# Optimization experiments

Measured on AMD Instinct MI355X. Metric: run time of the kernel, lower is better.

## Reference

```python
import jax, jax.numpy as jnp
import numpy as np

NUM_HEADS = 32
NUM_KV_HEADS = 8
HEAD_DIM = 128


def rotate_half(x):
    half = x.shape[-1] // 2
    return jnp.concatenate([-x[..., half:], x[..., :half]], axis=-1)


def setup_inputs() -> dict:
    key = jax.random.key(0)
    ks = jax.random.split(key, 7)
    B, S, H = 2, 2048, 4096
    hidden_states = jax.random.normal(ks[0], (B, S, H), dtype=jnp.float32)
    # rope tables built from real frequencies for realism
    inv_freq = 1.0 / (10000.0 ** (jnp.arange(0, HEAD_DIM, 2, dtype=jnp.float32) / HEAD_DIM))
    pos = jnp.arange(S, dtype=jnp.float32)
    freqs = pos[:, None] * inv_freq[None, :]            # [S, HEAD_DIM//2]
    emb = jnp.concatenate([freqs, freqs], axis=-1)      # [S, HEAD_DIM]
    cos = jnp.broadcast_to(jnp.cos(emb)[None], (B, S, HEAD_DIM)).astype(jnp.float32)
    sin = jnp.broadcast_to(jnp.sin(emb)[None], (B, S, HEAD_DIM)).astype(jnp.float32)
    scale = 0.02
    wq = jax.random.normal(ks[1], (NUM_HEADS * HEAD_DIM, H), dtype=jnp.float32) * scale
    wk = jax.random.normal(ks[2], (NUM_KV_HEADS * HEAD_DIM, H), dtype=jnp.float32) * scale
    wv = jax.random.normal(ks[3], (NUM_KV_HEADS * HEAD_DIM, H), dtype=jnp.float32) * scale
    wo = jax.random.normal(ks[4], (H, NUM_HEADS * HEAD_DIM), dtype=jnp.float32) * scale
    return {"hidden_states": hidden_states, "cos": cos, "sin": sin,
            "wq": wq, "wk": wk, "wv": wv, "wo": wo}


def reference(hidden_states, cos, sin, wq, wk, wv, wo):
    B, S, H = hidden_states.shape
    groups = NUM_HEADS // NUM_KV_HEADS
    scaling = HEAD_DIM ** -0.5

    # QKV projections (nn.Linear, no bias -> x @ W^T)
    q = (hidden_states @ wq.T).reshape(B, S, NUM_HEADS, HEAD_DIM).transpose(0, 2, 1, 3)     # [B,Hq,S,D]
    k = (hidden_states @ wk.T).reshape(B, S, NUM_KV_HEADS, HEAD_DIM).transpose(0, 2, 1, 3)  # [B,Hk,S,D]
    v = (hidden_states @ wv.T).reshape(B, S, NUM_KV_HEADS, HEAD_DIM).transpose(0, 2, 1, 3)  # [B,Hk,S,D]

    # RoPE (HF apply_rotary_pos_emb: cos/sin unsqueezed over head axis)
    c = cos[:, None, :, :]  # [B,1,S,D]
    s = sin[:, None, :, :]
    q = q * c + rotate_half(q) * s
    k = k * c + rotate_half(k) * s

    # GQA: broadcast each KV head to its group of query heads
    k = jnp.repeat(k, groups, axis=1)  # [B,Hq,S,D]
    v = jnp.repeat(v, groups, axis=1)

    # causal SDPA
    scores = jnp.einsum('bhqd,bhkd->bhqk', q, k) * scaling
    causal = jnp.tril(jnp.ones((S, S), dtype=bool))
    neg = jnp.finfo(scores.dtype).min
    scores = jnp.where(causal[None, None], scores, neg)
    probs = jax.nn.softmax(scores, axis=-1)
    attn = jnp.einsum('bhqk,bhkd->bhqd', probs, v)      # [B,Hq,S,D]

    # merge heads + output projection
    attn = attn.transpose(0, 2, 1, 3).reshape(B, S, NUM_HEADS * HEAD_DIM)
    return attn @ wo.T
```

## Files before the change

kernel.cpp:

```cpp
#include <hip/hip_runtime.h>
#include <stdint.h>

typedef __bf16 bf16_t;
typedef __bf16 bf16x8 __attribute__((ext_vector_type(8)));
typedef __bf16 bf16x4 __attribute__((ext_vector_type(4)));
typedef __bf16 bf16x2 __attribute__((ext_vector_type(2)));
typedef float f32x4 __attribute__((ext_vector_type(4)));

#define S_LEN 2048
#define NH 32
#define NKV 8
#define HD 128
#define B_SZ 2
#define HID 4096
#define QKV_N 6144
#define INFF __builtin_inff()
#define QSCALE (0.08838834764831845f * 1.4426950408889634f)

__device__ __forceinline__ void gload_lds16(const void* g, void* l) {
    __builtin_amdgcn_global_load_lds(
        (const __attribute__((address_space(1))) void*)(uintptr_t)g,
        (__attribute__((address_space(3))) void*)(uint32_t)(uintptr_t)l,
        16, 0, 0);
}

__global__ __launch_bounds__(256) void f2b_kernel(const float4* __restrict__ in,
                                                  bf16x4* __restrict__ out, int n4) {
    int i = blockIdx.x * blockDim.x + threadIdx.x;
    if (i >= n4) return;
    float4 v = in[i];
    bf16x4 o = {(bf16_t)v.x, (bf16_t)v.y, (bf16_t)v.z, (bf16_t)v.w};
    out[i] = o;
}

#define SLOT_E 16384

#define GTILE(T, STAGE, VMW) do {                                                         \
    const int _sb = ((T) & 3) * SLOT_E;                                                   \
    bf16x8 af[8], bfr[2];                                                                 \
    _Pragma("unroll") for (int i = 0; i < 8; ++i)                                         \
        af[i] = *(const bf16x8*)&lds[_sb + offA[i]];                                      \
    bfr[0] = *(const bf16x8*)&lds[_sb + 8192 + offB[0]];                                  \
    bfr[1] = *(const bf16x8*)&lds[_sb + 8192 + offB[1]];                                  \
    if (STAGE) {                                                                          \
        const int _ss = (((T) + 3) & 3) * SLOT_E;                                         \
        gload_lds16(sA0, &lds[_ss + ldsO0]); gload_lds16(sA1, &lds[_ss + ldsO1]);         \
        sA0 += 32; sA1 += 32;                                                             \
    }                                                                                     \
    __builtin_amdgcn_s_barrier();                                                         \
    asm volatile("s_waitcnt lgkmcnt(0)" ::: "memory");                                    \
    __builtin_amdgcn_sched_barrier(0);                                                    \
    __builtin_amdgcn_s_setprio(1);                                                        \
    _Pragma("unroll") for (int i = 0; i < 8; ++i) {                                       \
        acc[i][0] = __builtin_amdgcn_mfma_f32_16x16x32_bf16(af[i], bfr[0], acc[i][0], 0, 0, 0); \
        acc[i][1] = __builtin_amdgcn_mfma_f32_16x16x32_bf16(af[i], bfr[1], acc[i][1], 0, 0, 0); \
    }                                                                                     \
    __builtin_amdgcn_s_setprio(0);                                                        \
    __builtin_amdgcn_s_barrier();                                                         \
    bf16x8 bfs[2];                                                                        \
    bfs[0] = *(const bf16x8*)&lds[_sb + 8192 + offB[2]];                                  \
    bfs[1] = *(const bf16x8*)&lds[_sb + 8192 + offB[3]];                                  \
    if (STAGE) {                                                                          \
        const int _ss = (((T) + 3) & 3) * SLOT_E;                                         \
        gload_lds16(sB0, &lds[_ss + 8192 + ldsO0]); gload_lds16(sB1, &lds[_ss + 8192 + ldsO1]); \
        sB0 += 32; sB1 += 32;                                                             \
    }                                                                                     \
    __builtin_amdgcn_s_barrier();                                                         \
    asm volatile("s_waitcnt lgkmcnt(0)" ::: "memory");                                    \
    __builtin_amdgcn_sched_barrier(0);                                                    \
    __builtin_amdgcn_s_setprio(1);                                                        \
    _Pragma("unroll") for (int i = 0; i < 8; ++i) {                                       \
        acc[i][2] = __builtin_amdgcn_mfma_f32_16x16x32_bf16(af[i], bfs[0], acc[i][2], 0, 0, 0); \
        acc[i][3] = __builtin_amdgcn_mfma_f32_16x16x32_bf16(af[i], bfs[1], acc[i][3], 0, 0, 0); \
    }                                                                                     \
    __builtin_amdgcn_s_setprio(0);                                                        \
    if ((VMW) == 8)      asm volatile("s_waitcnt vmcnt(8)" ::: "memory");                 \
    else if ((VMW) == 4) asm volatile("s_waitcnt vmcnt(4)" ::: "memory");                 \
    else if ((VMW) == 0) asm volatile("s_waitcnt vmcnt(0)" ::: "memory");                 \
    __builtin_amdgcn_s_barrier();                                                         \
} while (0)

template<bool F32OUT>
__global__ __launch_bounds__(512, 2) void gemm256(const bf16_t* __restrict__ A,
                                                  const bf16_t* __restrict__ W,
                                                  void* __restrict__ C0,
                                                  void* __restrict__ C1,
                                                  int ld0, int ld1,
                                                  int Nloc, int ldAW, int Kloc) {
    __shared__ __align__(16) bf16_t lds[4 * SLOT_E];
    const int tid = threadIdx.x;
    const int lane = tid & 63;
    const int w = tid >> 6;
    const int wm = w >> 2, wn = w & 3;
    const int l15 = lane & 15, lg = lane >> 4;

    const int z = blockIdx.y;
    void* Cv = z ? C1 : C0;
    const int ldC = z ? ld1 : ld0;
    const int kOff = z * Kloc;

    const int nbx = Nloc >> 8;
    const int cpx = gridDim.x >> 3;
    const int bid = blockIdx.x;
    const int bid2 = (bid & 7) * cpx + (bid >> 3);
    const int m0 = (bid2 / nbx) * 256;
    const int n0 = (bid2 % nbx) * 256;

    const int c0 = tid, c1 = 512 + tid;
    const int rA0 = c0 >> 2, ch0 = (c0 & 3) ^ ((rA0 >> 1) & 3);
    const int rA1 = c1 >> 2, ch1 = (c1 & 3) ^ ((rA1 >> 1) & 3);
    const bf16_t* sA0 = A + (size_t)(m0 + rA0) * ldAW + kOff + ch0 * 8;
    const bf16_t* sA1 = A + (size_t)(m0 + rA1) * ldAW + kOff + ch1 * 8;
    const bf16_t* sB0 = W + (size_t)(n0 + rA0) * ldAW + kOff + ch0 * 8;
    const bf16_t* sB1 = W + (size_t)(n0 + rA1) * ldAW + kOff + ch1 * 8;
    const int ldsO0 = c0 * 8, ldsO1 = c1 * 8;

    int offA[8], offB[4];
    #pragma unroll
    for (int i = 0; i < 8; ++i) {
        int row = wm * 128 + i * 16 + l15;
        offA[i] = row * 32 + ((lg ^ ((row >> 1) & 3)) * 8);
    }
    #pragma unroll
    for (int j = 0; j < 4; ++j) {
        int row = wn * 64 + j * 16 + l15;
        offB[j] = row * 32 + ((lg ^ ((row >> 1) & 3)) * 8);
    }

    #pragma unroll
    for (int tt = 0; tt < 3; ++tt) {
        const int ss = tt * SLOT_E;
        gload_lds16(sA0, &lds[ss + ldsO0]); gload_lds16(sA1, &lds[ss + ldsO1]);
        gload_lds16(sB0, &lds[ss + 8192 + ldsO0]); gload_lds16(sB1, &lds[ss + 8192 + ldsO1]);
        sA0 += 32; sA1 += 32; sB0 += 32; sB1 += 32;
    }
    asm volatile("s_waitcnt vmcnt(8)" ::: "memory");
    __builtin_amdgcn_s_barrier();

    f32x4 acc[8][4] = {};
    const int NT = Kloc >> 5;
    int t = 0;
    for (; t < NT - 3; ++t) GTILE(t, true, 8);
    GTILE(NT - 3, false, 4);
    GTILE(NT - 2, false, 0);
    GTILE(NT - 1, false, -1);

    #pragma unroll
    for (int i = 0; i < 8; ++i)
        #pragma unroll
        for (int jn = 0; jn < 4; ++jn)
            #pragma unroll
            for (int r = 0; r < 4; ++r) {
                int m = m0 + wm * 128 + i * 16 + lg * 4 + r;
                int n = n0 + wn * 64 + jn * 16 + l15;
                float v = acc[i][jn][r];
                if (F32OUT) ((float*)Cv)[(size_t)m * ldC + n] = v;
                else        ((bf16_t*)Cv)[(size_t)m * ldC + n] = (bf16_t)v;
            }
}

__global__ __launch_bounds__(256) void rope_fuse(bf16_t* __restrict__ QKV,
                                                 const bf16_t* __restrict__ P1,
                                                 const float* __restrict__ cosb,
                                                 const float* __restrict__ sinb) {
    int tid = blockIdx.x * blockDim.x + threadIdx.x;
    int d = tid & 63;
    int hg = (tid >> 6) % 48;
    int bs = tid / (64 * 48);
    bf16_t* rowp;
    float x1, x2, posc = 1.f;
    if (hg < 32) {
        rowp = QKV + (size_t)bs * QKV_N + hg * HD;
        x1 = (float)rowp[d];
        x2 = (float)rowp[d + 64];
        posc = QSCALE;
    } else if (hg < 40) {
        int col = HID + (hg - 32) * HD;
        rowp = QKV + (size_t)bs * QKV_N + col;
        const bf16_t* pp = P1 + (size_t)bs * 2048 + (col - HID);
        x1 = (float)rowp[d] + (float)pp[d];
        x2 = (float)rowp[d + 64] + (float)pp[d + 64];
    } else {
        int col = HID + NKV * HD + (hg - 40) * HD;
        rowp = QKV + (size_t)bs * QKV_N + col;
        const bf16_t* pp = P1 + (size_t)bs * 2048 + (col - HID);
        rowp[d]      = (bf16_t)((float)rowp[d]      + (float)pp[d]);
        rowp[d + 64] = (bf16_t)((float)rowp[d + 64] + (float)pp[d + 64]);
        return;
    }
    float c1 = cosb[(size_t)bs * HD + d];
    float s1 = sinb[(size_t)bs * HD + d];
    float c2 = cosb[(size_t)bs * HD + d + 64];
    float s2 = sinb[(size_t)bs * HD + d + 64];
    rowp[d]      = (bf16_t)((x1 * c1 - x2 * s1) * posc);
    rowp[d + 64] = (bf16_t)((x2 * c2 + x1 * s2) * posc);
}

#define PITCH_P 72

__global__ __launch_bounds__(512, 2) void attn_fwd(const bf16_t* __restrict__ QKV,
                                                   bf16_t* __restrict__ O) {
    __shared__ __align__(16) bf16_t Kl[64 * 128];
    __shared__ __align__(16) bf16_t Vt[128 * 64];
    __shared__ __align__(16) bf16_t Pl[8][16 * PITCH_P];
    const int tid = threadIdx.x;
    const int lane = tid & 63;
    const int w = tid >> 6;
    const int l15 = lane & 15, lg = lane >> 4;
    const int pr = blockIdx.x, kvh = blockIdx.y, b = blockIdx.z;
    const int h = kvh * 4 + (w & 3);
    const int rg = w >> 2;

    int krow[2], kch[2];
    #pragma unroll
    for (int jj = 0; jj < 2; ++jj) { int q = jj * 512 + tid; krow[jj] = q >> 4; kch[jj] = q & 15; }
    const int k0v = (tid & 31) * 2;
    const int d0 = (tid >> 5) * 8;
    const int vci = k0v >> 3;
    const int vsub = k0v & 7;

    const bf16_t* Kb0 = QKV + (size_t)(b * S_LEN) * QKV_N + HID + kvh * HD;
    const bf16_t* Vb0 = QKV + (size_t)(b * S_LEN) * QKV_N + HID + NKV * HD + kvh * HD;
    bf16_t* Plw = Pl[w];

    for (int t = 0; t < 2; ++t) {
        const int qt = (t == 0) ? pr : (63 - pr);
        const int q0 = qt * 32;
        const int qrow = q0 + rg * 16 + l15;

        bf16x8 qf[4];
        {
            const bf16_t* qp = QKV + (size_t)(b * S_LEN + qrow) * QKV_N + h * HD;
            #pragma unroll
            for (int c = 0; c < 4; ++c) qf[c] = *(const bf16x8*)&qp[c * 32 + lg * 8];
        }

        f32x4 acc_o[8] = {};
        float mrow = -INFF, lrow = 0.f;
        const int nsteps = qt / 2 + 1;

        bf16x8 kst[2], vst[2];
        #pragma unroll
        for (int jj = 0; jj < 2; ++jj)
            kst[jj] = *(const bf16x8*)&Kb0[(size_t)krow[jj] * QKV_N + kch[jj] * 8];
        vst[0] = *(const bf16x8*)&Vb0[(size_t)(k0v + 0) * QKV_N + d0];
        vst[1] = *(const bf16x8*)&Vb0[(size_t)(k0v + 1) * QKV_N + d0];

        for (int st = 0; st < nsteps; ++st) {
            const int k0 = st * 64;
            __syncthreads();
            #pragma unroll
            for (int jj = 0; jj < 2; ++jj)
                *(bf16x8*)&Kl[krow[jj] * 128 + ((kch[jj] ^ (krow[jj] & 7)) * 8)] = kst[jj];
            #pragma unroll
            for (int j = 0; j < 8; ++j) {
                bf16x2 v2 = { vst[0][j], vst[1][j] };
                *(bf16x2*)&Vt[(d0 + j) * 64 + ((vci ^ j) << 3) + vsub] = v2;
            }
            __syncthreads();
            if (st + 1 < nsteps) {
                const bf16_t* Kb = Kb0 + (size_t)(k0 + 64) * QKV_N;
                const bf16_t* Vb = Vb0 + (size_t)(k0 + 64) * QKV_N;
                #pragma unroll
                for (int jj = 0; jj < 2; ++jj)
                    kst[jj] = *(const bf16x8*)&Kb[(size_t)krow[jj] * QKV_N + kch[jj] * 8];
                vst[0] = *(const bf16x8*)&Vb[(size_t)(k0v + 0) * QKV_N + d0];
                vst[1] = *(const bf16x8*)&Vb[(size_t)(k0v + 1) * QKV_N + d0];
            }
            f32x4 s[4];
            __builtin_amdgcn_s_setprio(1);
            #pragma unroll
            for (int nt = 0; nt < 4; ++nt) {
                s[nt] = (f32x4){0.f, 0.f, 0.f, 0.f};
                const int row = nt * 16 + l15;
                const int rb = row * 128, key = row & 7;
                #pragma unroll
                for (int c = 0; c < 4; ++c) {
                    bf16x8 kf = *(const bf16x8*)&Kl[rb + (((c * 4 + lg) ^ key) * 8)];
                    s[nt] = __builtin_amdgcn_mfma_f32_16x16x32_bf16(kf, qf[c], s[nt], 0, 0, 0);
                }
            }
            __builtin_amdgcn_s_setprio(0);
            if (k0 + 63 > q0 + rg * 16) {
                #pragma unroll
                for (int nt = 0; nt < 4; ++nt)
                    #pragma unroll
                    for (int r = 0; r < 4; ++r) {
                        int k = k0 + nt * 16 + lg * 4 + r;
                        if (k > qrow) s[nt][r] = -INFF;
                    }
            }
            float m0a = fmaxf(fmaxf(s[0][0], s[0][1]), fmaxf(s[0][2], s[0][3]));
            float m1a = fmaxf(fmaxf(s[1][0], s[1][1]), fmaxf(s[1][2], s[1][3]));
            float m2a = fmaxf(fmaxf(s[2][0], s[2][1]), fmaxf(s[2][2], s[2][3]));
            float m3a = fmaxf(fmaxf(s[3][0], s[3][1]), fmaxf(s[3][2], s[3][3]));
            float mx = fmaxf(fmaxf(m0a, m1a), fmaxf(m2a, m3a));
            mx = fmaxf(mx, __shfl_xor(mx, 16));
            mx = fmaxf(mx, __shfl_xor(mx, 32));
            const bool nodefer = !__all(mx <= mrow + 11.5f);
            const float mn = nodefer ? fmaxf(mrow, mx) : mrow;
            float sc = 1.f;
            if (nodefer) sc = exp2f(mrow - mn);
            float rs0 = 0.f, rs1 = 0.f, rs2 = 0.f, rs3 = 0.f;
            #pragma unroll
            for (int nt = 0; nt < 4; ++nt) {
                float e0 = exp2f(s[nt][0] - mn), e1 = exp2f(s[nt][1] - mn);
                float e2 = exp2f(s[nt][2] - mn), e3 = exp2f(s[nt][3] - mn);
                s[nt][0] = e0; s[nt][1] = e1; s[nt][2] = e2; s[nt][3] = e3;
                rs0 += e0; rs1 += e1; rs2 += e2; rs3 += e3;
            }
            float rs = (rs0 + rs1) + (rs2 + rs3);
            rs += __shfl_xor(rs, 16);
            rs += __shfl_xor(rs, 32);
            if (nodefer) { lrow = lrow * sc + rs; mrow = mn; }
            else         { lrow += rs; }
            #pragma unroll
            for (int nt = 0; nt < 4; ++nt) {
                bf16x4 pk = {(bf16_t)s[nt][0], (bf16_t)s[nt][1], (bf16_t)s[nt][2], (bf16_t)s[nt][3]};
                *(bf16x4*)&Plw[l15 * PITCH_P + nt * 16 + lg * 4] = pk;
            }
            if (nodefer) {
                float scb[4];
                #pragma unroll
                for (int r = 0; r < 4; ++r) scb[r] = __shfl(sc, lg * 4 + r);
                #pragma unroll
                for (int nt2 = 0; nt2 < 8; ++nt2)
                    #pragma unroll
                    for (int r = 0; r < 4; ++r) acc_o[nt2][r] *= scb[r];
            }
            __builtin_amdgcn_s_setprio(1);
            #pragma unroll
            for (int kc = 0; kc < 2; ++kc) {
                bf16x8 pf = *(const bf16x8*)&Plw[l15 * PITCH_P + kc * 32 + lg * 8];
                #pragma unroll
                for (int nt2 = 0; nt2 < 8; ++nt2) {
                    const int drow = nt2 * 16 + l15;
                    bf16x8 vf = *(const bf16x8*)&Vt[drow * 64 + (((kc * 4 + lg) ^ (drow & 7)) << 3)];
                    acc_o[nt2] = __builtin_amdgcn_mfma_f32_16x16x32_bf16(pf, vf, acc_o[nt2], 0, 0, 0);
                }
            }
            __builtin_amdgcn_s_setprio(0);
        }
        float lb[4];
        #pragma unroll
        for (int r = 0; r < 4; ++r) lb[r] = __builtin_amdgcn_rcpf(__shfl(lrow, lg * 4 + r));
        #pragma unroll
        for (int nt2 = 0; nt2 < 8; ++nt2)
            #pragma unroll
            for (int r = 0; r < 4; ++r) {
                int q = q0 + rg * 16 + lg * 4 + r;
                int d = nt2 * 16 + l15;
                O[((size_t)(b * S_LEN + q)) * (NH * HD) + h * HD + d] = (bf16_t)(acc_o[nt2][r] * lb[r]);
            }
        __syncthreads();
    }
}

extern "C" void kernel_launch(void* const* d_in, const int* in_sizes, int n_in,
                              void* d_out, int out_size, void* d_ws, size_t ws_size,
                              hipStream_t stream) {
    const float* hs   = (const float*)d_in[0];
    const float* cosb = (const float*)d_in[1];
    const float* sinb = (const float*)d_in[2];
    const float* wq   = (const float*)d_in[3];
    const float* wk   = (const float*)d_in[4];
    const float* wv   = (const float*)d_in[5];
    const float* wo   = (const float*)d_in[6];
    float* out = (float*)d_out;

    const size_t NHS = (size_t)B_SZ * S_LEN * HID;
    const size_t NQKVW = (size_t)QKV_N * HID;
    size_t need = (NHS * 3 + NQKVW * 2) * sizeof(bf16_t);
    if (ws_size < need) return;

    bf16_t* p = (bf16_t*)d_ws;
    bf16_t* hsb  = p; p += NHS;
    bf16_t* wqkv = p; p += NQKVW;
    bf16_t* wob  = p; p += NHS;
    bf16_t* QKVb = p; p += NQKVW;
    bf16_t* Ab   = p; p += NHS;
    bf16_t* P1   = Ab;

    auto cvt = [&](const float* src, bf16_t* dst, size_t n) {
        int n4 = (int)(n / 4);
        f2b_kernel<<<(n4 + 255) / 256, 256, 0, stream>>>((const float4*)src, (bf16x4*)dst, n4);
    };
    cvt(hs, hsb, NHS);
    cvt(wq, wqkv, NHS);
    cvt(wk, wqkv + (size_t)HID * HID, (size_t)NKV * HD * HID);
    cvt(wv, wqkv + (size_t)(HID + NKV * HD) * HID, (size_t)NKV * HD * HID);
    cvt(wo, wob, NHS);

    gemm256<false><<<dim3(256, 1), 512, 0, stream>>>(hsb, wqkv, QKVb, QKVb,
                                                     QKV_N, QKV_N, 4096, HID, HID);
    gemm256<false><<<dim3(128, 2), 512, 0, stream>>>(hsb, wqkv + (size_t)HID * HID,
                                                     QKVb + HID, P1,
                                                     QKV_N, 2048, 2048, HID, 2048);

    int rf_threads = B_SZ * S_LEN * 48 * 64;
    rope_fuse<<<rf_threads / 256, 256, 0, stream>>>(QKVb, P1, cosb, sinb);

    attn_fwd<<<dim3(32, NKV, B_SZ), 512, 0, stream>>>(QKVb, Ab);

    gemm256<true><<<dim3(256, 1), 512, 0, stream>>>(Ab, wob, out, out,
                                                    HID, HID, HID, HID, HID);
}
```

Before: 549.9 us.

## Process two query row-blocks per wave in attention with double-buffered K/V LDS

Each wave now handles 32 query rows (two 16-row MFMA tiles) against the same K/V tile, doubling the query tile per block to 64 and halving the grid. K/V shared-memory tiles are double-buffered, so one of the two barriers per step is removed. This reuses each K/V LDS load across twice as many MFMAs to cut LDS traffic and sync overhead. In exchange it raises register pressure (dropped min-blocks launch bound), grows LDS use, and leaves fewer blocks (256) to fill the GPU.

```diff
diff --git a/kernel.cpp b/kernel.cpp
--- a/kernel.cpp
+++ b/kernel.cpp
@@ -198,11 +198,11 @@
 
 #define PITCH_P 72
 
-__global__ __launch_bounds__(512, 2) void attn_fwd(const bf16_t* __restrict__ QKV,
-                                                   bf16_t* __restrict__ O) {
-    __shared__ __align__(16) bf16_t Kl[64 * 128];
-    __shared__ __align__(16) bf16_t Vt[128 * 64];
-    __shared__ __align__(16) bf16_t Pl[8][16 * PITCH_P];
+__global__ __launch_bounds__(512) void attn_fwd(const bf16_t* __restrict__ QKV,
+                                                bf16_t* __restrict__ O) {
+    __shared__ __align__(16) bf16_t Kl[2][64 * 128];
+    __shared__ __align__(16) bf16_t Vt[2][128 * 64];
+    __shared__ __align__(16) bf16_t Pl[8][2][16 * PITCH_P];
     const int tid = threadIdx.x;
     const int lane = tid & 63;
     const int w = tid >> 6;
@@ -221,23 +221,30 @@
 
     const bf16_t* Kb0 = QKV + (size_t)(b * S_LEN) * QKV_N + HID + kvh * HD;
     const bf16_t* Vb0 = QKV + (size_t)(b * S_LEN) * QKV_N + HID + NKV * HD + kvh * HD;
-    bf16_t* Plw = Pl[w];
+    bf16_t* Pl0 = Pl[w][0];
+    bf16_t* Pl1 = Pl[w][1];
 
     for (int t = 0; t < 2; ++t) {
-        const int qt = (t == 0) ? pr : (63 - pr);
-        const int q0 = qt * 32;
-        const int qrow = q0 + rg * 16 + l15;
-
-        bf16x8 qf[4];
+        const int qt = (t == 0) ? pr : (31 - pr);
+        const int q0 = qt * 64;
+        const int qb0 = q0 + rg * 32;
+        const int qb1 = qb0 + 16;
+        const int qrow0 = qb0 + l15, qrow1 = qb1 + l15;
+
+        bf16x8 qf0[4], qf1[4];
         {
-            const bf16_t* qp = QKV + (size_t)(b * S_LEN + qrow) * QKV_N + h * HD;
-            #pragma unroll
-            for (int c = 0; c < 4; ++c) qf[c] = *(const bf16x8*)&qp[c * 32 + lg * 8];
+            const bf16_t* qp0 = QKV + (size_t)(b * S_LEN + qrow0) * QKV_N + h * HD;
+            const bf16_t* qp1 = QKV + (size_t)(b * S_LEN + qrow1) * QKV_N + h * HD;
+            #pragma unroll
+            for (int c = 0; c < 4; ++c) {
+                qf0[c] = *(const bf16x8*)&qp0[c * 32 + lg * 8];
+                qf1[c] = *(const bf16x8*)&qp1[c * 32 + lg * 8];
+            }
         }
 
-        f32x4 acc_o[8] = {};
-        float mrow = -INFF, lrow = 0.f;
-        const int nsteps = qt / 2 + 1;
+        f32x4 acc0[8] = {}, acc1[8] = {};
+        float mr0 = -INFF, lr0 = 0.f, mr1 = -INFF, lr1 = 0.f;
+        const int nsteps = qt + 1;
 
         bf16x8 kst[2], vst[2];
         #pragma unroll
@@ -248,14 +255,14 @@
 
         for (int st = 0; st < nsteps; ++st) {
             const int k0 = st * 64;
-            __syncthreads();
+            const int p = st & 1;
             #pragma unroll
             for (int jj = 0; jj < 2; ++jj)
-                *(bf16x8*)&Kl[krow[jj] * 128 + ((kch[jj] ^ (krow[jj] & 7)) * 8)] = kst[jj];
+                *(bf16x8*)&Kl[p][krow[jj] * 128 + ((kch[jj] ^ (krow[jj] & 7)) * 8)] = kst[jj];
             #pragma unroll
             for (int j = 0; j < 8; ++j) {
                 bf16x2 v2 = { vst[0][j], vst[1][j] };
-                *(bf16x2*)&Vt[(d0 + j) * 64 + ((vci ^ j) << 3) + vsub] = v2;
+                *(bf16x2*)&Vt[p][(d0 + j) * 64 + ((vci ^ j) << 3) + vsub] = v2;
             }
             __syncthreads();
             if (st + 1 < nsteps) {
@@ -267,90 +274,148 @@
                 vst[0] = *(const bf16x8*)&Vb[(size_t)(k0v + 0) * QKV_N + d0];
                 vst[1] = *(const bf16x8*)&Vb[(size_t)(k0v + 1) * QKV_N + d0];
             }
-            f32x4 s[4];
+            f32x4 s0[4], s1[4];
             __builtin_amdgcn_s_setprio(1);
             #pragma unroll
             for (int nt = 0; nt < 4; ++nt) {
-                s[nt] = (f32x4){0.f, 0.f, 0.f, 0.f};
+                s0[nt] = (f32x4){0.f, 0.f, 0.f, 0.f};
+                s1[nt] = (f32x4){0.f, 0.f, 0.f, 0.f};
                 const int row = nt * 16 + l15;
                 const int rb = row * 128, key = row & 7;
                 #pragma unroll
                 for (int c = 0; c < 4; ++c) {
-                    bf16x8 kf = *(const bf16x8*)&Kl[rb + (((c * 4 + lg) ^ key) * 8)];
-                    s[nt] = __builtin_amdgcn_mfma_f32_16x16x32_bf16(kf, qf[c], s[nt], 0, 0, 0);
+                    bf16x8 kf = *(const bf16x8*)&Kl[p][rb + (((c * 4 + lg) ^ key) * 8)];
+                    s0[nt] = __builtin_amdgcn_mfma_f32_16x16x32_bf16(kf, qf0[c], s0[nt], 0, 0, 0);
+                    s1[nt] = __builtin_amdgcn_mfma_f32_16x16x32_bf16(kf, qf1[c], s1[nt], 0, 0, 0);
                 }
             }
             __builtin_amdgcn_s_setprio(0);
-            if (k0 + 63 > q0 + rg * 16) {
+            if (k0 + 63 > qb0) {
                 #pragma unroll
                 for (int nt = 0; nt < 4; ++nt)
                     #pragma unroll
                     for (int r = 0; r < 4; ++r) {
                         int k = k0 + nt * 16 + lg * 4 + r;
-                        if (k > qrow) s[nt][r] = -INFF;
+                        if (k > qrow0) s0[nt][r] = -INFF;
                     }
             }
-            float m0a = fmaxf(fmaxf(s[0][0], s[0][1]), fmaxf(s[0][2], s[0][3]));
-            float m1a = fmaxf(fmaxf(s[1][0], s[1][1]), fmaxf(s[1][2], s[1][3]));
-            float m2a = fmaxf(fmaxf(s[2][0], s[2][1]), fmaxf(s[2][2], s[2][3]));
-            float m3a = fmaxf(fmaxf(s[3][0], s[3][1]), fmaxf(s[3][2], s[3][3]));
-            float mx = fmaxf(fmaxf(m0a, m1a), fmaxf(m2a, m3a));
-            mx = fmaxf(mx, __shfl_xor(mx, 16));
-            mx = fmaxf(mx, __shfl_xor(mx, 32));
-            const bool nodefer = !__all(mx <= mrow + 11.5f);
-            const float mn = nodefer ? fmaxf(mrow, mx) : mrow;
-            float sc = 1.f;
-            if (nodefer) sc = exp2f(mrow - mn);
-            float rs0 = 0.f, rs1 = 0.f, rs2 = 0.f, rs3 = 0.f;
-            #pragma unroll
-            for (int nt = 0; nt < 4; ++nt) {
-                float e0 = exp2f(s[nt][0] - mn), e1 = exp2f(s[nt][1] - mn);
-                float e2 = exp2f(s[nt][2] - mn), e3 = exp2f(s[nt][3] - mn);
-                s[nt][0] = e0; s[nt][1] = e1; s[nt][2] = e2; s[nt][3] = e3;
-                rs0 += e0; rs1 += e1; rs2 += e2; rs3 += e3;
-            }
-            float rs = (rs0 + rs1) + (rs2 + rs3);
-            rs += __shfl_xor(rs, 16);
-            rs += __shfl_xor(rs, 32);
-            if (nodefer) { lrow = lrow * sc + rs; mrow = mn; }
-            else         { lrow += rs; }
-            #pragma unroll
-            for (int nt = 0; nt < 4; ++nt) {
-                bf16x4 pk = {(bf16_t)s[nt][0], (bf16_t)s[nt][1], (bf16_t)s[nt][2], (bf16_t)s[nt][3]};
-                *(bf16x4*)&Plw[l15 * PITCH_P + nt * 16 + lg * 4] = pk;
-            }
-            if (nodefer) {
-                float scb[4];
-                #pragma unroll
-                for (int r = 0; r < 4; ++r) scb[r] = __shfl(sc, lg * 4 + r);
-                #pragma unroll
-                for (int nt2 = 0; nt2 < 8; ++nt2)
-                    #pragma unroll
-                    for (int r = 0; r < 4; ++r) acc_o[nt2][r] *= scb[r];
+            if (k0 + 63 > qb1) {
+                #pragma unroll
+                for (int nt = 0; nt < 4; ++nt)
+                    #pragma unroll
+                    for (int r = 0; r < 4; ++r) {
+                        int k = k0 + nt * 16 + lg * 4 + r;
+                        if (k > qrow1) s1[nt][r] = -INFF;
+                    }
+            }
+            {
+                float ma = fmaxf(fmaxf(s0[0][0], s0[0][1]), fmaxf(s0[0][2], s0[0][3]));
+                float mb = fmaxf(fmaxf(s0[1][0], s0[1][1]), fmaxf(s0[1][2], s0[1][3]));
+                float mc = fmaxf(fmaxf(s0[2][0], s0[2][1]), fmaxf(s0[2][2], s0[2][3]));
+                float md = fmaxf(fmaxf(s0[3][0], s0[3][1]), fmaxf(s0[3][2], s0[3][3]));
+                float mx = fmaxf(fmaxf(ma, mb), fmaxf(mc, md));
+                mx = fmaxf(mx, __shfl_xor(mx, 16));
+                mx = fmaxf(mx, __shfl_xor(mx, 32));
+                const bool nodefer = !__all(mx <= mr0 + 11.5f);
+                const float mn = nodefer ? fmaxf(mr0, mx) : mr0;
+                float sc = 1.f;
+                if (nodefer) sc = exp2f(mr0 - mn);
+                float rsum = 0.f;
+                #pragma unroll
+                for (int nt = 0; nt < 4; ++nt) {
+                    float e0 = exp2f(s0[nt][0] - mn), e1 = exp2f(s0[nt][1] - mn);
+                    float e2 = exp2f(s0[nt][2] - mn), e3 = exp2f(s0[nt][3] - mn);
+                    s0[nt][0] = e0; s0[nt][1] = e1; s0[nt][2] = e2; s0[nt][3] = e3;
+                    rsum += (e0 + e1) + (e2 + e3);
+                }
+                rsum += __shfl_xor(rsum, 16);
+                rsum += __shfl_xor(rsum, 32);
+                if (nodefer) { lr0 = lr0 * sc + rsum; mr0 = mn; }
+                else         { lr0 += rsum; }
+                #pragma unroll
+                for (int nt = 0; nt < 4; ++nt) {
+                    bf16x4 pk = {(bf16_t)s0[nt][0], (bf16_t)s0[nt][1], (bf16_t)s0[nt][2], (bf16_t)s0[nt][3]};
+                    *(bf16x4*)&Pl0[l15 * PITCH_P + nt * 16 + lg * 4] = pk;
+                }
+                if (nodefer) {
+                    float scb[4];
+                    #pragma unroll
+                    for (int r = 0; r < 4; ++r) scb[r] = __shfl(sc, lg * 4 + r);
+                    #pragma unroll
+                    for (int nt2 = 0; nt2 < 8; ++nt2)
+                        #pragma unroll
+                        for (int r = 0; r < 4; ++r) acc0[nt2][r] *= scb[r];
+                }
+            }
+            {
+                float ma = fmaxf(fmaxf(s1[0][0], s1[0][1]), fmaxf(s1[0][2], s1[0][3]));
+                float mb = fmaxf(fmaxf(s1[1][0], s1[1][1]), fmaxf(s1[1][2], s1[1][3]));
+                float mc = fmaxf(fmaxf(s1[2][0], s1[2][1]), fmaxf(s1[2][2], s1[2][3]));
+                float md = fmaxf(fmaxf(s1[3][0], s1[3][1]), fmaxf(s1[3][2], s1[3][3]));
+                float mx = fmaxf(fmaxf(ma, mb), fmaxf(mc, md));
+                mx = fmaxf(mx, __shfl_xor(mx, 16));
+                mx = fmaxf(mx, __shfl_xor(mx, 32));
+                const bool nodefer = !__all(mx <= mr1 + 11.5f);
+                const float mn = nodefer ? fmaxf(mr1, mx) : mr1;
+                float sc = 1.f;
+                if (nodefer) sc = exp2f(mr1 - mn);
+                float rsum = 0.f;
+                #pragma unroll
+                for (int nt = 0; nt < 4; ++nt) {
+                    float e0 = exp2f(s1[nt][0] - mn), e1 = exp2f(s1[nt][1] - mn);
+                    float e2 = exp2f(s1[nt][2] - mn), e3 = exp2f(s1[nt][3] - mn);
+                    s1[nt][0] = e0; s1[nt][1] = e1; s1[nt][2] = e2; s1[nt][3] = e3;
+                    rsum += (e0 + e1) + (e2 + e3);
+                }
+                rsum += __shfl_xor(rsum, 16);
+                rsum += __shfl_xor(rsum, 32);
+                if (nodefer) { lr1 = lr1 * sc + rsum; mr1 = mn; }
+                else         { lr1 += rsum; }
+                #pragma unroll
+                for (int nt = 0; nt < 4; ++nt) {
+                    bf16x4 pk = {(bf16_t)s1[nt][0], (bf16_t)s1[nt][1], (bf16_t)s1[nt][2], (bf16_t)s1[nt][3]};
+                    *(bf16x4*)&Pl1[l15 * PITCH_P + nt * 16 + lg * 4] = pk;
+                }
+                if (nodefer) {
+                    float scb[4];
+                    #pragma unroll
+                    for (int r = 0; r < 4; ++r) scb[r] = __shfl(sc, lg * 4 + r);
+                    #pragma unroll
+                    for (int nt2 = 0; nt2 < 8; ++nt2)
+                        #pragma unroll
+                        for (int r = 0; r < 4; ++r) acc1[nt2][r] *= scb[r];
+                }
             }
             __builtin_amdgcn_s_setprio(1);
             #pragma unroll
             for (int kc = 0; kc < 2; ++kc) {
-                bf16x8 pf = *(const bf16x8*)&Plw[l15 * PITCH_P + kc * 32 + lg * 8];
+                bf16x8 pf0 = *(const bf16x8*)&Pl0[l15 * PITCH_P + kc * 32 + lg * 8];
+                bf16x8 pf1 = *(const bf16x8*)&Pl1[l15 * PITCH_P + kc * 32 + lg * 8];
                 #pragma unroll
                 for (int nt2 = 0; nt2 < 8; ++nt2) {
                     const int drow = nt2 * 16 + l15;
-                    bf16x8 vf = *(const bf16x8*)&Vt[drow * 64 + (((kc * 4 + lg) ^ (drow & 7)) << 3)];
-                    acc_o[nt2] = __builtin_amdgcn_mfma_f32_16x16x32_bf16(pf, vf, acc_o[nt2], 0, 0, 0);
+                    bf16x8 vf = *(const bf16x8*)&Vt[p][drow * 64 + (((kc * 4 + lg) ^ (drow & 7)) << 3)];
+                    acc0[nt2] = __builtin_amdgcn_mfma_f32_16x16x32_bf16(pf0, vf, acc0[nt2], 0, 0, 0);
+                    acc1[nt2] = __builtin_amdgcn_mfma_f32_16x16x32_bf16(pf1, vf, acc1[nt2], 0, 0, 0);
                 }
             }
             __builtin_amdgcn_s_setprio(0);
         }
-        float lb[4];
+        float lb0[4], lb1[4];
         #pragma unroll
-        for (int r = 0; r < 4; ++r) lb[r] = __builtin_amdgcn_rcpf(__shfl(lrow, lg * 4 + r));
+        for (int r = 0; r < 4; ++r) {
+            lb0[r] = __builtin_amdgcn_rcpf(__shfl(lr0, lg * 4 + r));
+            lb1[r] = __builtin_amdgcn_rcpf(__shfl(lr1, lg * 4 + r));
+        }
         #pragma unroll
         for (int nt2 = 0; nt2 < 8; ++nt2)
             #pragma unroll
             for (int r = 0; r < 4; ++r) {
-                int q = q0 + rg * 16 + lg * 4 + r;
                 int d = nt2 * 16 + l15;
-                O[((size_t)(b * S_LEN + q)) * (NH * HD) + h * HD + d] = (bf16_t)(acc_o[nt2][r] * lb[r]);
+                int qa = qb0 + lg * 4 + r;
+                int qb = qb1 + lg * 4 + r;
+                O[((size_t)(b * S_LEN + qa)) * (NH * HD) + h * HD + d] = (bf16_t)(acc0[nt2][r] * lb0[r]);
+                O[((size_t)(b * S_LEN + qb)) * (NH * HD) + h * HD + d] = (bf16_t)(acc1[nt2][r] * lb1[r]);
             }
         __syncthreads();
     }
@@ -400,7 +465,7 @@
     int rf_threads = B_SZ * S_LEN * 48 * 64;
     rope_fuse<<<rf_threads / 256, 256, 0, stream>>>(QKVb, P1, cosb, sinb);
 
-    attn_fwd<<<dim3(32, NKV, B_SZ), 512, 0, stream>>>(QKVb, Ab);
+    attn_fwd<<<dim3(16, NKV, B_SZ), 512, 0, stream>>>(QKVb, Ab);
 
     gemm256<true><<<dim3(256, 1), 512, 0, stream>>>(Ab, wob, out, out,
                                                     HID, HID, HID, HID, HID);
```

Measured after the change: 525.4 us. -4.4%, faster.
